# Kernel optimization log

Hardware: AMD Instinct MI355X
Metric: run time of the kernel (lower is better)

The kernel has to match this reference:

```python
import jax, jax.numpy as jnp
import numpy as np

EPS = 1e-6

def _resize_mask_nearest(mask, h, w):
    # mask: (B, H, W) float in {0,1} -> (B, 1, h, w), F.interpolate mode='nearest' semantics
    B, H, W = mask.shape
    ih = (jnp.arange(h) * H) // h  # floor(dst * H/h)
    iw = (jnp.arange(w) * W) // w
    m = mask[:, ih][:, :, iw]
    return m[:, None]  # (B,1,h,w)

def masked_avg_pool(feat, mask_rs):
    # feat: (B,C,H,W), mask_rs: (B,1,H,W) -> (B,C)
    num = (feat * mask_rs).sum(axis=(2, 3))
    den = mask_rs.sum(axis=(2, 3)) + EPS
    return num / den

def compute_P(proto_fg, proto_bg, R):
    # proto_*: (B,d); R: (2,d) learnable anchors -> P: (B,d,d)
    B, d = proto_fg.shape
    C = jnp.stack([proto_bg, proto_fg], axis=1)                     # (B,2,d)
    C = C / (jnp.sqrt((C ** 2).sum(axis=2, keepdims=True)) + EPS)
    Rn = R / (jnp.sqrt((R ** 2).sum(axis=1, keepdims=True)) + EPS)  # (2,d)
    Rb = jnp.broadcast_to(Rn[None], (B, 2, d))
    P = jnp.matmul(jnp.linalg.pinv(C), Rb)                          # (B,d,d)
    return jnp.swapaxes(P, 1, 2)

def apply_P_to_feat(P, feat):
    b, d, h, w = feat.shape
    out = jnp.einsum('bij,bjn->bin', P, feat.reshape(b, d, h * w))
    return out.reshape(b, d, h, w)

def masked_topk_tokens(feat, mask_rs, k):
    # feat: (B,C,H,W), mask_rs: (B,1,H,W) -> tokens (B,k,C); deterministic L2-norm top-k
    b, c, h, w = feat.shape
    scores = jnp.sqrt((feat ** 2).sum(axis=1)).reshape(b, -1)       # (B,HW)
    mask_flat = mask_rs.reshape(b, -1)
    valid = mask_flat.sum(axis=1) > 0
    mask_flat = jnp.where(valid[:, None], mask_flat, 1.0)           # fallback_to_full
    scores = jnp.where(mask_flat >= 0.5, scores, -jnp.inf)
    _, idx = jax.lax.top_k(scores, k)                               # (B,k)
    tok = jnp.take_along_axis(feat.reshape(b, c, -1), idx[:, None, :], axis=2)  # (B,C,k)
    return jnp.swapaxes(tok, 1, 2)                                  # (B,k,C)

def setup_inputs() -> dict:
    key = jax.random.key(0)
    ks = jax.random.split(key, 12)
    B, d = 8, 256
    sizes = [(64, 64), (32, 32), (16, 16)]
    inp = {}
    for i, (h, w) in enumerate(sizes):
        inp[f'q{i+1}'] = jax.random.normal(ks[i], (B, d, h, w), jnp.float32)
        inp[f's{i+1}'] = jax.random.normal(ks[3 + i], (B, d, h, w), jnp.float32)
        # kaiming_normal fan_in=d, linear -> std = 1/sqrt(d)
        inp[f'r{i+1}'] = jax.random.normal(ks[6 + i], (2, d), jnp.float32) / jnp.sqrt(jnp.float32(d))
    inp['support_mask'] = jax.random.randint(ks[9], (B, 512, 512), 0, 2, jnp.int32)
    inp['k'] = 32
    return inp

def reference(q1, q2, q3, s1, s2, s3, r1, r2, r3, support_mask, k):
    mask = support_mask.astype(jnp.float32)  # (B,H,W)
    qs = [q1, q2, q3]
    ss = [s1, s2, s3]
    rs = [r1, r2, r3]
    parts_q, parts_s, pfgs, pbgs = [], [], [], []
    mask_rs0 = None
    s_t0 = None
    for li in range(3):
        q, s, R = qs[li], ss[li], rs[li]
        b, d, h, w = s.shape
        mask_rs = _resize_mask_nearest(mask, h, w)
        proto_fg = masked_avg_pool(s, mask_rs)
        proto_bg = masked_avg_pool(s, 1.0 - mask_rs)
        P = compute_P(proto_fg, proto_bg, R)
        q_t = apply_P_to_feat(P, q)
        s_t = apply_P_to_feat(P, s)
        parts_q.append(q_t.reshape(b, d, -1))
        parts_s.append(s_t.reshape(b, d, -1))
        pfgs.append(masked_avg_pool(s_t, mask_rs))
        pbgs.append(masked_avg_pool(s_t, 1.0 - mask_rs))
        if li == 0:
            mask_rs0, s_t0 = mask_rs, s_t
    tokens = masked_topk_tokens(s_t0, mask_rs0, k)  # (B,k,d)
    # pack everything into one (B, d, N) array: q_t flats, s_t flats, fg/bg protos, tokens
    packed = jnp.concatenate(
        parts_q + parts_s
        + [jnp.stack(pfgs, axis=2), jnp.stack(pbgs, axis=2), jnp.swapaxes(tokens, 1, 2)],
        axis=2)
    return packed
```

## Files before the change

kernel.cpp:

```cpp
#include <hip/hip_runtime.h>
#include <math.h>

#define NTOT 10790
#define EPSF 1e-6f

__device__ __forceinline__ float block_reduce_sum(float v, float* red) {
    int tid = threadIdx.x;
    red[tid] = v; __syncthreads();
    for (int off = 128; off > 0; off >>= 1) {
        if (tid < off) red[tid] += red[tid + off];
        __syncthreads();
    }
    float r = red[0];
    __syncthreads();
    return r;
}

__device__ __forceinline__ bool kvGreater(float as, int ai, float bs, int bi) {
    return (as > bs) || (as == bs && ai < bi);
}

__device__ __forceinline__ void sort64(float& s, int& i, int lane) {
    #pragma unroll
    for (int k = 2; k <= 64; k <<= 1) {
        #pragma unroll
        for (int j = k >> 1; j > 0; j >>= 1) {
            float os = __shfl_xor(s, j, 64);
            int   oi = __shfl_xor(i, j, 64);
            bool lower = (lane & j) == 0;
            bool blockDesc = (lane & k) == 0;
            bool keepG = (blockDesc == lower);
            bool og = kvGreater(os, oi, s, i);
            if (og == keepG) { s = os; i = oi; }
        }
    }
}

__device__ __forceinline__ void merge64(float& as, int& ai, float bs, int bi, int lane) {
    float rbs = __shfl(bs, 63 - lane, 64);
    int   rbi = __shfl(bi, 63 - lane, 64);
    if (!kvGreater(as, ai, rbs, rbi)) { as = rbs; ai = rbi; }
    #pragma unroll
    for (int j = 32; j > 0; j >>= 1) {
        float os = __shfl_xor(as, j, 64);
        int   oi = __shfl_xor(ai, j, 64);
        bool lower = (lane & j) == 0;
        bool og = kvGreater(os, oi, as, ai);
        if (og == lower) { as = os; ai = oi; }
    }
}

__global__ __launch_bounds__(256) void mask_kernel(const int* __restrict__ mask,
                                                   float* __restrict__ wsm0,
                                                   float* __restrict__ wsm1,
                                                   float* __restrict__ wsm2,
                                                   float* __restrict__ msum) {
    int level = blockIdx.x, b = blockIdx.y, tid = threadIdx.x;
    int h = 64 >> level, w = h, S = 8 << level, HW = h * w;
    float* wsm = (level == 0) ? wsm0 : ((level == 1) ? wsm1 : wsm2);
    const int* mb = mask + (size_t)b * 512 * 512;
    float acc = 0.f;
    for (int n = tid; n < HW; n += 256) {
        int y = n / w, x = n - y * w;
        float mv = (float)mb[y * S * 512 + x * S];
        wsm[b * HW + n] = mv;
        acc += mv;
    }
    __shared__ float red[256];
    float s = block_reduce_sum(acc, red);
    if (tid == 0) msum[b * 3 + level] = s;
}

__global__ __launch_bounds__(256) void sreduce_kernel(const float* __restrict__ s0,
                                                      const float* __restrict__ s1,
                                                      const float* __restrict__ s2,
                                                      const float* __restrict__ wsm0,
                                                      const float* __restrict__ wsm1,
                                                      const float* __restrict__ wsm2,
                                                      float* __restrict__ fgnum,
                                                      float* __restrict__ tot) {
    int c = blockIdx.x, b = blockIdx.y, level = blockIdx.z, tid = threadIdx.x;
    int HW = 4096 >> (2 * level);
    const float* s = (level == 0) ? s0 : ((level == 1) ? s1 : s2);
    const float* wsm = (level == 0) ? wsm0 : ((level == 1) ? wsm1 : wsm2);
    const float* sb = s + ((size_t)(b * 256) + c) * HW;
    const float* mb = wsm + b * HW;
    float af = 0.f, at = 0.f;
    for (int n = tid; n < HW; n += 256) {
        float x = sb[n];
        float m = mb[n];
        at += x;
        af = fmaf(x, m, af);
    }
    __shared__ float redA[256], redB[256];
    redA[tid] = af; redB[tid] = at; __syncthreads();
    for (int off = 128; off > 0; off >>= 1) {
        if (tid < off) { redA[tid] += redA[tid + off]; redB[tid] += redB[tid + off]; }
        __syncthreads();
    }
    if (tid == 0) {
        int base = (level * 8 + b) * 256 + c;
        fgnum[base] = redA[0];
        tot[base]   = redB[0];
    }
}

__global__ __launch_bounds__(256) void protos_kernel(const float* __restrict__ R0p,
                                                     const float* __restrict__ R1p,
                                                     const float* __restrict__ R2p,
                                                     const float* __restrict__ fgnum,
                                                     const float* __restrict__ tot,
                                                     const float* __restrict__ msum,
                                                     float* __restrict__ c0v,
                                                     float* __restrict__ c1v,
                                                     float* __restrict__ rn0v,
                                                     float* __restrict__ rn1v,
                                                     float* __restrict__ minv,
                                                     float* __restrict__ rg) {
    int b = blockIdx.x, level = blockIdx.y, c = threadIdx.x;
    int HW = 4096 >> (2 * level);
    const float* R = (level == 0) ? R0p : ((level == 1) ? R1p : R2p);
    __shared__ float red[256];
    int base = (level * 8 + b) * 256;
    float ms = msum[b * 3 + level];
    float denf = ms + EPSF;
    float denb = ((float)HW - ms) + EPSF;
    float fg = fgnum[base + c];
    float tt = tot[base + c];
    float pf = fg / denf;
    float pb = (tt - fg) / denb;
    float nf = block_reduce_sum(pf * pf, red);
    float nb = block_reduce_sum(pb * pb, red);
    float C1 = pf / (sqrtf(nf) + EPSF);
    float C0 = pb / (sqrtf(nb) + EPSF);
    c0v[base + c] = C0;
    c1v[base + c] = C1;
    float r0 = R[c], r1 = R[256 + c];
    float n0 = block_reduce_sum(r0 * r0, red);
    float n1 = block_reduce_sum(r1 * r1, red);
    float rr = block_reduce_sum(r0 * r1, red);
    float i0 = 1.0f / (sqrtf(n0) + EPSF);
    float i1 = 1.0f / (sqrtf(n1) + EPSF);
    rn0v[base + c] = r0 * i0;
    rn1v[base + c] = r1 * i1;
    float a  = block_reduce_sum(C0 * C0, red);
    float bb = block_reduce_sum(C0 * C1, red);
    float cc = block_reduce_sum(C1 * C1, red);
    if (c == 0) {
        float det = a * cc - bb * bb;
        float id = 1.0f / det;
        float* M = minv + (level * 8 + b) * 4;
        M[0] = cc * id; M[1] = -bb * id; M[2] = -bb * id; M[3] = a * id;
        float* G = rg + (level * 8 + b) * 4;
        G[0] = n0 * i0 * i0;
        G[1] = rr * i0 * i1;
        G[2] = n1 * i1 * i1;
    }
}

__global__ __launch_bounds__(256) void transform_kernel(const float* __restrict__ q0,
                                                        const float* __restrict__ q1,
                                                        const float* __restrict__ q2,
                                                        const float* __restrict__ s0,
                                                        const float* __restrict__ s1,
                                                        const float* __restrict__ s2,
                                                        float* __restrict__ out,
                                                        const float* __restrict__ c0v,
                                                        const float* __restrict__ c1v,
                                                        const float* __restrict__ rn0v,
                                                        const float* __restrict__ rn1v,
                                                        const float* __restrict__ minv,
                                                        const float* __restrict__ wsm0,
                                                        const float* __restrict__ wsm1,
                                                        const float* __restrict__ wsm2,
                                                        float* __restrict__ vbuf,
                                                        float* __restrict__ partials) {
    int b = blockIdx.y;
    int xb = blockIdx.x;
    int is_s = (xb >= 84);
    if (is_s) xb -= 84;
    int level, blk;
    if (xb < 64)      { level = 0; blk = xb; }
    else if (xb < 80) { level = 1; blk = xb - 64; }
    else              { level = 2; blk = xb - 80; }
    int HW = 4096 >> (2 * level);
    const float* x = is_s ? ((level == 0) ? s0 : ((level == 1) ? s1 : s2))
                          : ((level == 0) ? q0 : ((level == 1) ? q1 : q2));
    const float* wsm = (level == 0) ? wsm0 : ((level == 1) ? wsm1 : wsm2);
    const int qoffs[3] = {0, 4096, 5120};
    const int soffs[3] = {5376, 9472, 10496};
    int col_off = is_s ? soffs[level] : qoffs[level];

    int n0 = blk * 64;
    int tid = threadIdx.x;
    int p = tid & 63, g = tid >> 6;
    __shared__ float sc0[256], sc1[256], srn0[256], srn1[256];
    __shared__ float st0[4][64], st1[4][64];
    __shared__ float su0[64], su1[64];
    int base = (level * 8 + b) * 256;
    sc0[tid] = c0v[base + tid];
    sc1[tid] = c1v[base + tid];
    srn0[tid] = rn0v[base + tid];
    srn1[tid] = rn1v[base + tid];
    __syncthreads();

    const float* xb_ptr = x + (size_t)(b * 256) * HW;
    int n = n0 + p;
    float t0 = 0.f, t1 = 0.f;
    #pragma unroll 8
    for (int i = 0; i < 64; i++) {
        int c = g * 64 + i;
        float xv = xb_ptr[(size_t)c * HW + n];
        t0 = fmaf(sc0[c], xv, t0);
        t1 = fmaf(sc1[c], xv, t1);
    }
    st0[g][p] = t0; st1[g][p] = t1;
    __syncthreads();

    if (tid < 64) {
        float a0 = st0[0][p] + st0[1][p] + st0[2][p] + st0[3][p];
        float a1 = st1[0][p] + st1[1][p] + st1[2][p] + st1[3][p];
        const float* M = minv + (level * 8 + b) * 4;
        float u0 = M[0] * a0 + M[1] * a1;
        float u1 = M[1] * a0 + M[3] * a1;
        su0[p] = u0; su1[p] = u1;
        if (is_s && level == 0) {
            *(float2*)&vbuf[((size_t)b * 4096 + n) * 2] = make_float2(u0, u1);
        }
        if (is_s) {
            float m = wsm[b * HW + n];
            float s0r = m * u0, s1r = m * u1, s2r = u0, s3r = u1;
            for (int off = 32; off > 0; off >>= 1) {
                s0r += __shfl_down(s0r, off, 64);
                s1r += __shfl_down(s1r, off, 64);
                s2r += __shfl_down(s2r, off, 64);
                s3r += __shfl_down(s3r, off, 64);
            }
            if (p == 0) {
                float* pp = partials + (((level * 8 + b) * 64) + blk) * 4;
                pp[0] = s0r; pp[1] = s1r; pp[2] = s2r; pp[3] = s3r;
            }
        }
    }
    __syncthreads();

    float* ob = out + (size_t)(b * 256) * NTOT + col_off + n0;
    #pragma unroll 8
    for (int i = 0; i < 64; i++) {
        int c = g * 64 + i;
        ob[(size_t)c * NTOT + p] = fmaf(srn0[c], su0[p], srn1[c] * su1[p]);
    }
}

__global__ __launch_bounds__(256) void protoT_kernel(float* __restrict__ out,
                                                     const float* __restrict__ partials,
                                                     const float* __restrict__ rn0v,
                                                     const float* __restrict__ rn1v,
                                                     const float* __restrict__ msum) {
    int b = blockIdx.x, level = blockIdx.y, tid = threadIdx.x;
    const int HWs[3] = {4096, 1024, 256};
    const int nblks[3] = {64, 16, 4};
    __shared__ float A[4];
    if (tid == 0) {
        float s0 = 0, s1 = 0, s2 = 0, s3 = 0;
        const float* pp = partials + ((size_t)(level * 8 + b) * 64) * 4;
        int nb = nblks[level];
        for (int i = 0; i < nb; i++) {
            s0 += pp[i * 4 + 0]; s1 += pp[i * 4 + 1];
            s2 += pp[i * 4 + 2]; s3 += pp[i * 4 + 3];
        }
        float ms = msum[b * 3 + level];
        float denf = ms + EPSF;
        float denb = ((float)HWs[level] - ms) + EPSF;
        A[0] = s0 / denf;
        A[1] = s1 / denf;
        A[2] = (s2 - s0) / denb;
        A[3] = (s3 - s1) / denb;
    }
    __syncthreads();
    int base = (level * 8 + b) * 256;
    float r0 = rn0v[base + tid], r1 = rn1v[base + tid];
    size_t row = ((size_t)(b * 256) + tid) * NTOT;
    out[row + 10752 + level] = fmaf(r0, A[0], r1 * A[1]);
    out[row + 10755 + level] = fmaf(r0, A[2], r1 * A[3]);
}

__global__ __launch_bounds__(1024) void topk_kernel(float* __restrict__ out,
                                                    const float* __restrict__ v,
                                                    const float* __restrict__ wsm0,
                                                    const float* __restrict__ msum,
                                                    const float* __restrict__ rn0v,
                                                    const float* __restrict__ rn1v,
                                                    const float* __restrict__ rg) {
    int b = blockIdx.x, tid = threadIdx.x;
    int w = tid >> 6, lane = tid & 63;
    __shared__ float lds_s[16 * 64];
    __shared__ int   lds_i[16 * 64];
    __shared__ float2 suv[32];

    float A = rg[b * 4 + 0], B = rg[b * 4 + 1], C = rg[b * 4 + 2];
    bool validmask = msum[b * 3 + 0] > 0.0f;

    float as; int ai;
    #pragma unroll
    for (int c4 = 0; c4 < 4; ++c4) {
        int n = (w * 4 + c4) * 64 + lane;
        float2 uv = *(const float2*)&v[((size_t)b * 4096 + n) * 2];
        float ss = fmaxf(A * uv.x * uv.x + 2.0f * B * uv.x * uv.y + C * uv.y * uv.y, 0.0f);
        float s = sqrtf(ss);
        float m = validmask ? wsm0[b * 4096 + n] : 1.0f;
        s = (m >= 0.5f) ? s : -INFINITY;
        int i = n;
        sort64(s, i, lane);
        if (c4 == 0) { as = s; ai = i; }
        else merge64(as, ai, s, i, lane);
    }
    lds_s[w * 64 + lane] = as;
    lds_i[w * 64 + lane] = ai;
    __syncthreads();

    for (int act = 8; act >= 1; act >>= 1) {
        float ms_; int mi_;
        bool active = (w < act);
        if (active) {
            ms_ = lds_s[(2 * w) * 64 + lane];
            mi_ = lds_i[(2 * w) * 64 + lane];
            float bs_ = lds_s[(2 * w + 1) * 64 + lane];
            int   bi_ = lds_i[(2 * w + 1) * 64 + lane];
            merge64(ms_, mi_, bs_, bi_, lane);
        }
        __syncthreads();
        if (active) {
            lds_s[w * 64 + lane] = ms_;
            lds_i[w * 64 + lane] = mi_;
        }
        __syncthreads();
    }

    if (tid < 32) {
        int idx = lds_i[tid];
        suv[tid] = *(const float2*)&v[((size_t)b * 4096 + idx) * 2];
    }
    __syncthreads();

    int c = tid & 255, j4 = tid >> 8;
    float r0 = rn0v[b * 256 + c], r1 = rn1v[b * 256 + c];
    size_t row = ((size_t)(b * 256) + c) * NTOT + 10758;
    #pragma unroll
    for (int t = 0; t < 8; ++t) {
        int j = j4 * 8 + t;
        float2 uv = suv[j];
        out[row + j] = fmaf(r0, uv.x, r1 * uv.y);
    }
}

extern "C" void kernel_launch(void* const* d_in, const int* in_sizes, int n_in,
                              void* d_out, int out_size, void* d_ws, size_t ws_size,
                              hipStream_t stream) {
    const float* q0 = (const float*)d_in[0];
    const float* s0 = (const float*)d_in[1];
    const float* r0 = (const float*)d_in[2];
    const float* q1 = (const float*)d_in[3];
    const float* s1 = (const float*)d_in[4];
    const float* r1 = (const float*)d_in[5];
    const float* q2 = (const float*)d_in[6];
    const float* s2 = (const float*)d_in[7];
    const float* r2 = (const float*)d_in[8];
    const int* mask = (const int*)d_in[9];
    float* out = (float*)d_out;
    float* W = (float*)d_ws;

    float* wsm0 = W;
    float* wsm1 = W + 32768;
    float* wsm2 = W + 40960;
    float* msum = W + 43008;
    float* fgnum = W + 43040;
    float* tot  = W + 49184;
    float* c0v  = W + 55328;
    float* c1v  = W + 61472;
    float* rn0v = W + 67616;
    float* rn1v = W + 73760;
    float* minv = W + 79904;
    float* rg   = W + 80000;
    float* vbuf = W + 80128;
    float* part = W + 145664;

    mask_kernel<<<dim3(3, 8), 256, 0, stream>>>(mask, wsm0, wsm1, wsm2, msum);

    sreduce_kernel<<<dim3(256, 8, 3), 256, 0, stream>>>(s0, s1, s2, wsm0, wsm1, wsm2,
                                                        fgnum, tot);

    protos_kernel<<<dim3(8, 3), 256, 0, stream>>>(r0, r1, r2, fgnum, tot, msum,
                                                  c0v, c1v, rn0v, rn1v, minv, rg);

    transform_kernel<<<dim3(168, 8), 256, 0, stream>>>(q0, q1, q2, s0, s1, s2, out,
                                                       c0v, c1v, rn0v, rn1v, minv,
                                                       wsm0, wsm1, wsm2, vbuf, part);

    protoT_kernel<<<dim3(8, 3), 256, 0, stream>>>(out, part, rn0v, rn1v, msum);

    topk_kernel<<<8, 1024, 0, stream>>>(out, vbuf, wsm0, msum, rn0v, rn1v, rg);
}
```

Baseline: 86.99 us.

## Vectorize loads and stores in sreduce, transform and topk kernels

```diff
diff --git a/kernel.cpp b/kernel.cpp
--- a/kernel.cpp
+++ b/kernel.cpp
@@ -2,6 +2,7 @@
 #include <math.h>
 
 #define NTOT 10790
+#define NTOT2 5395
 #define EPSF 1e-6f
 
 __device__ __forceinline__ float block_reduce_sum(float v, float* red) {
@@ -81,16 +82,17 @@
                                                       float* __restrict__ tot) {
     int c = blockIdx.x, b = blockIdx.y, level = blockIdx.z, tid = threadIdx.x;
     int HW = 4096 >> (2 * level);
+    int HW4 = HW >> 2;
     const float* s = (level == 0) ? s0 : ((level == 1) ? s1 : s2);
     const float* wsm = (level == 0) ? wsm0 : ((level == 1) ? wsm1 : wsm2);
-    const float* sb = s + ((size_t)(b * 256) + c) * HW;
-    const float* mb = wsm + b * HW;
+    const float4* sb4 = (const float4*)(s + ((size_t)(b * 256) + c) * HW);
+    const float4* mb4 = (const float4*)(wsm + (size_t)b * HW);
     float af = 0.f, at = 0.f;
-    for (int n = tid; n < HW; n += 256) {
-        float x = sb[n];
-        float m = mb[n];
-        at += x;
-        af = fmaf(x, m, af);
+    for (int i = tid; i < HW4; i += 256) {
+        float4 x = sb4[i];
+        float4 m = mb4[i];
+        at += (x.x + x.y) + (x.z + x.w);
+        af = fmaf(x.x, m.x, fmaf(x.y, m.y, fmaf(x.z, m.z, fmaf(x.w, m.w, af))));
     }
     __shared__ float redA[256], redB[256];
     redA[tid] = af; redB[tid] = at; __syncthreads();
@@ -177,26 +179,27 @@
                                                         float* __restrict__ partials) {
     int b = blockIdx.y;
     int xb = blockIdx.x;
-    int is_s = (xb >= 84);
-    if (is_s) xb -= 84;
+    int is_s = (xb >= 42);
+    if (is_s) xb -= 42;
     int level, blk;
-    if (xb < 64)      { level = 0; blk = xb; }
-    else if (xb < 80) { level = 1; blk = xb - 64; }
-    else              { level = 2; blk = xb - 80; }
+    if (xb < 32)      { level = 0; blk = xb; }
+    else if (xb < 40) { level = 1; blk = xb - 32; }
+    else              { level = 2; blk = xb - 40; }
     int HW = 4096 >> (2 * level);
+    int HW4 = HW >> 2;
     const float* x = is_s ? ((level == 0) ? s0 : ((level == 1) ? s1 : s2))
                           : ((level == 0) ? q0 : ((level == 1) ? q1 : q2));
     const float* wsm = (level == 0) ? wsm0 : ((level == 1) ? wsm1 : wsm2);
     const int qoffs[3] = {0, 4096, 5120};
     const int soffs[3] = {5376, 9472, 10496};
     int col_off = is_s ? soffs[level] : qoffs[level];
-
-    int n0 = blk * 64;
+    int n0 = blk * 128;
     int tid = threadIdx.x;
-    int p = tid & 63, g = tid >> 6;
+
     __shared__ float sc0[256], sc1[256], srn0[256], srn1[256];
-    __shared__ float st0[4][64], st1[4][64];
-    __shared__ float su0[64], su1[64];
+    __shared__ float st0[8][32][4], st1[8][32][4];
+    __shared__ float4 su4[64];
+    __shared__ float pred[2][4];
     int base = (level * 8 + b) * 256;
     sc0[tid] = c0v[base + tid];
     sc1[tid] = c1v[base + tid];
@@ -204,30 +207,44 @@
     srn1[tid] = rn1v[base + tid];
     __syncthreads();
 
-    const float* xb_ptr = x + (size_t)(b * 256) * HW;
-    int n = n0 + p;
-    float t0 = 0.f, t1 = 0.f;
+    const float4* xb4 = (const float4*)(x + (size_t)(b * 256) * HW);
+    int cg = tid >> 5, l = tid & 31;
+    size_t idx0 = (size_t)(cg * 32) * HW4 + (n0 >> 2) + l;
+    float t0x = 0, t0y = 0, t0z = 0, t0w = 0;
+    float t1x = 0, t1y = 0, t1z = 0, t1w = 0;
     #pragma unroll 8
-    for (int i = 0; i < 64; i++) {
-        int c = g * 64 + i;
-        float xv = xb_ptr[(size_t)c * HW + n];
-        t0 = fmaf(sc0[c], xv, t0);
-        t1 = fmaf(sc1[c], xv, t1);
-    }
-    st0[g][p] = t0; st1[g][p] = t1;
-    __syncthreads();
-
-    if (tid < 64) {
-        float a0 = st0[0][p] + st0[1][p] + st0[2][p] + st0[3][p];
-        float a1 = st1[0][p] + st1[1][p] + st1[2][p] + st1[3][p];
+    for (int i = 0; i < 32; i++) {
+        int c = cg * 32 + i;
+        float4 xv = xb4[idx0 + (size_t)i * HW4];
+        float a = sc0[c], bq = sc1[c];
+        t0x = fmaf(a, xv.x, t0x); t0y = fmaf(a, xv.y, t0y);
+        t0z = fmaf(a, xv.z, t0z); t0w = fmaf(a, xv.w, t0w);
+        t1x = fmaf(bq, xv.x, t1x); t1y = fmaf(bq, xv.y, t1y);
+        t1z = fmaf(bq, xv.z, t1z); t1w = fmaf(bq, xv.w, t1w);
+    }
+    st0[cg][l][0] = t0x; st0[cg][l][1] = t0y; st0[cg][l][2] = t0z; st0[cg][l][3] = t0w;
+    st1[cg][l][0] = t1x; st1[cg][l][1] = t1y; st1[cg][l][2] = t1z; st1[cg][l][3] = t1w;
+    __syncthreads();
+
+    if (tid < 128) {
+        int p = tid;
+        const float* f0 = &st0[0][p >> 2][p & 3];
+        const float* f1 = &st1[0][p >> 2][p & 3];
+        float a0 = 0.f, a1 = 0.f;
+        #pragma unroll
+        for (int g2 = 0; g2 < 8; g2++) {
+            a0 += f0[g2 * 128];
+            a1 += f1[g2 * 128];
+        }
         const float* M = minv + (level * 8 + b) * 4;
         float u0 = M[0] * a0 + M[1] * a1;
         float u1 = M[1] * a0 + M[3] * a1;
-        su0[p] = u0; su1[p] = u1;
-        if (is_s && level == 0) {
-            *(float2*)&vbuf[((size_t)b * 4096 + n) * 2] = make_float2(u0, u1);
-        }
+        ((float2*)su4)[p] = make_float2(u0, u1);
         if (is_s) {
+            int n = n0 + p;
+            if (level == 0) {
+                *(float2*)&vbuf[((size_t)b * 4096 + n) * 2] = make_float2(u0, u1);
+            }
             float m = wsm[b * HW + n];
             float s0r = m * u0, s1r = m * u1, s2r = u0, s3r = u1;
             for (int off = 32; off > 0; off >>= 1) {
@@ -236,19 +253,32 @@
                 s2r += __shfl_down(s2r, off, 64);
                 s3r += __shfl_down(s3r, off, 64);
             }
-            if (p == 0) {
-                float* pp = partials + (((level * 8 + b) * 64) + blk) * 4;
-                pp[0] = s0r; pp[1] = s1r; pp[2] = s2r; pp[3] = s3r;
+            if ((tid & 63) == 0) {
+                int wv = tid >> 6;
+                pred[wv][0] = s0r; pred[wv][1] = s1r;
+                pred[wv][2] = s2r; pred[wv][3] = s3r;
             }
         }
     }
     __syncthreads();
-
-    float* ob = out + (size_t)(b * 256) * NTOT + col_off + n0;
+    if (is_s && tid == 0) {
+        float* pp = partials + (((level * 8 + b) * 64) + blk) * 4;
+        pp[0] = pred[0][0] + pred[1][0];
+        pp[1] = pred[0][1] + pred[1][1];
+        pp[2] = pred[0][2] + pred[1][2];
+        pp[3] = pred[0][3] + pred[1][3];
+    }
+
+    int g = tid >> 6, slot = tid & 63;
+    float4 sq = su4[slot];
+    float2* ob2 = (float2*)out + ((size_t)(b * 256) + g * 64) * NTOT2
+                  + ((col_off + n0) >> 1) + slot;
     #pragma unroll 8
     for (int i = 0; i < 64; i++) {
         int c = g * 64 + i;
-        ob[(size_t)c * NTOT + p] = fmaf(srn0[c], su0[p], srn1[c] * su1[p]);
+        float r0 = srn0[c], r1 = srn1[c];
+        ob2[(size_t)i * NTOT2] = make_float2(fmaf(r0, sq.x, r1 * sq.y),
+                                             fmaf(r0, sq.z, r1 * sq.w));
     }
 }
 
@@ -259,7 +289,7 @@
                                                      const float* __restrict__ msum) {
     int b = blockIdx.x, level = blockIdx.y, tid = threadIdx.x;
     const int HWs[3] = {4096, 1024, 256};
-    const int nblks[3] = {64, 16, 4};
+    const int nblks[3] = {32, 8, 2};
     __shared__ float A[4];
     if (tid == 0) {
         float s0 = 0, s1 = 0, s2 = 0, s3 = 0;
@@ -343,14 +373,15 @@
     }
     __syncthreads();
 
-    int c = tid & 255, j4 = tid >> 8;
+    int c = tid >> 2, qd = tid & 3;
     float r0 = rn0v[b * 256 + c], r1 = rn1v[b * 256 + c];
-    size_t row = ((size_t)(b * 256) + c) * NTOT + 10758;
+    float2* o2 = (float2*)out + ((size_t)(b * 256) + c) * NTOT2 + 5379 + qd * 4;
     #pragma unroll
-    for (int t = 0; t < 8; ++t) {
-        int j = j4 * 8 + t;
-        float2 uv = suv[j];
-        out[row + j] = fmaf(r0, uv.x, r1 * uv.y);
+    for (int t = 0; t < 4; ++t) {
+        float2 uv0 = suv[qd * 8 + 2 * t];
+        float2 uv1 = suv[qd * 8 + 2 * t + 1];
+        o2[t] = make_float2(fmaf(r0, uv0.x, r1 * uv0.y),
+                            fmaf(r0, uv1.x, r1 * uv1.y));
     }
 }
 
@@ -393,9 +424,9 @@
     protos_kernel<<<dim3(8, 3), 256, 0, stream>>>(r0, r1, r2, fgnum, tot, msum,
                                                   c0v, c1v, rn0v, rn1v, minv, rg);
 
-    transform_kernel<<<dim3(168, 8), 256, 0, stream>>>(q0, q1, q2, s0, s1, s2, out,
-                                                       c0v, c1v, rn0v, rn1v, minv,
-                                                       wsm0, wsm1, wsm2, vbuf, part);
+    transform_kernel<<<dim3(84, 8), 256, 0, stream>>>(q0, q1, q2, s0, s1, s2, out,
+                                                      c0v, c1v, rn0v, rn1v, minv,
+                                                      wsm0, wsm1, wsm2, vbuf, part);
 
     protoT_kernel<<<dim3(8, 3), 256, 0, stream>>>(out, part, rn0v, rn1v, msum);
 
```

After: 78.06 us. 10.3% less time.
